# Performance work log

Hardware: AMD Instinct MI355X
Metric: run time of the kernel (lower is better)

## Reference

```python
import jax, jax.numpy as jnp
import numpy as np

N = 300000      # total points
B = 4           # scenes
C_IN = 64
C_OUT = 128
GRID = 0.5      # voxel size
M = 128         # per-axis voxel index bound (10m / 0.5m = 20 << 128); key fits int32
EPS = 1e-5      # BatchNorm eps


def setup_inputs() -> dict:
    key = jax.random.key(0)
    k1, k2, k3 = jax.random.split(key, 3)
    coord = jax.random.uniform(k1, (N, 3), jnp.float32) * 10.0
    feat = jax.random.normal(k2, (N, C_IN), jnp.float32)
    offset = jnp.array([N // 4, N // 2, 3 * N // 4, N], jnp.int32)  # cumulative counts
    W = jax.random.normal(k3, (C_IN, C_OUT), jnp.float32) * 0.05    # fc weight (no bias)
    gamma = jnp.ones((C_OUT,), jnp.float32)
    beta = jnp.zeros((C_OUT,), jnp.float32)
    return {"coord": coord, "feat": feat, "offset": offset, "W": W, "gamma": gamma, "beta": beta}


def reference(coord, feat, offset, W, gamma, beta):
    n = coord.shape[0]
    # offset2batch: point i belongs to scene searchsorted(offset, i, 'right')
    batch = jnp.searchsorted(offset, jnp.arange(n, dtype=offset.dtype), side='right')
    # fc -> BatchNorm1d (training-mode batch stats, biased var) -> ReLU
    x = feat @ W                                    # [n, C_OUT]
    mean = x.mean(axis=0)
    var = x.var(axis=0)
    x = jax.nn.relu(gamma * (x - mean) * jax.lax.rsqrt(var + EPS) + beta)
    # start = per-scene min coordinate (segment_csr min)
    start = jax.ops.segment_min(coord, batch, num_segments=B)      # [B, 3]
    # voxel_grid: integer voxel index per point, hashed injectively with batch id
    v = jnp.floor((coord - start[batch]) / GRID).astype(jnp.int32)  # [n, 3]
    vkey = ((batch.astype(jnp.int32) * M + v[:, 0]) * M + v[:, 1]) * M + v[:, 2]
    # unique(sorted) with inverse/counts; padded to n for static shapes
    uniq, cluster, counts = jnp.unique(vkey, return_inverse=True, return_counts=True,
                                       size=n, fill_value=-1)
    cluster = cluster.reshape(-1)                   # [n] cluster id per point
    # segment mean of coords, segment max of features (padded segments -> 0)
    cnt = jnp.maximum(counts, 1).astype(coord.dtype)
    coord_out = jax.ops.segment_sum(coord, cluster, num_segments=n) / cnt[:, None]
    fmax = jax.ops.segment_max(x, cluster, num_segments=n)
    feat_out = jnp.where(counts[:, None] > 0, fmax, jnp.zeros((), x.dtype))
    # batch id of each cluster (clusters never cross scenes)
    batch_out = jax.ops.segment_min(batch, cluster, num_segments=n)
    return coord_out, feat_out, cluster, counts, batch_out
```

## Files before the change

### kernel.cpp

```cpp
#include <hip/hip_runtime.h>
#include <stdint.h>

#define CIN   64
#define COUT  128
#define EPSB  1e-5f
#define NWORDS2 4096
#define MAXNC 32768
#define SLABW 17

typedef short bf16x8 __attribute__((ext_vector_type(8)));
typedef float f32x4  __attribute__((ext_vector_type(4)));
typedef unsigned u32x4 __attribute__((ext_vector_type(4)));

__device__ __forceinline__ int batch_of(int i, const int* __restrict__ off, int B) {
    int b = 0;
    for (int j = 0; j < B - 1; ++j) b += (i >= off[j]) ? 1 : 0;
    return b;
}

__device__ __forceinline__ unsigned enc(float x) {
    unsigned b = __float_as_uint(x);
    return (b & 0x80000000u) ? ~b : (b | 0x80000000u);
}
__device__ __forceinline__ float dec(unsigned u) {
    unsigned b = (u & 0x80000000u) ? (u ^ 0x80000000u) : ~u;
    return __uint_as_float(b);
}

__device__ __forceinline__ unsigned short rne_bf16(float f) {
    unsigned u = __float_as_uint(f);
    unsigned r = u + 0x7FFFu + ((u >> 16) & 1u);
    return (unsigned short)(r >> 16);
}

__device__ __forceinline__ void split8(float4 A, float4 B, bf16x8& hi, bf16x8& lo) {
    float fs[8] = {A.x, A.y, A.z, A.w, B.x, B.y, B.z, B.w};
    u32x4 hv, lv;
    #pragma unroll
    for (int w = 0; w < 4; ++w) {
        float a = fs[2*w], b = fs[2*w+1];
        unsigned ua = __float_as_uint(a), ub = __float_as_uint(b);
        hv[w] = __builtin_amdgcn_perm(ub, ua, 0x07060302u);
        float la = a - __uint_as_float(ua & 0xFFFF0000u);
        float lb = b - __uint_as_float(ub & 0xFFFF0000u);
        lv[w] = __builtin_amdgcn_perm(__float_as_uint(lb), __float_as_uint(la), 0x07060302u);
    }
    hi = __builtin_bit_cast(bf16x8, hv);
    lo = __builtin_bit_cast(bf16x8, lv);
}

__global__ void k_init(float* __restrict__ coordOut, float* __restrict__ batchOut, int n,
                       unsigned* __restrict__ pooledU, int* __restrict__ countsWs,
                       unsigned* __restrict__ flags, int* __restrict__ sceneMin, int nScene,
                       const float* __restrict__ W, unsigned short* __restrict__ Wb)
{
    long i = (long)blockIdx.x * blockDim.x + threadIdx.x;
    long stride = (long)gridDim.x * blockDim.x;
    for (long t = i; t < 3L * n; t += stride) coordOut[t] = 0.f;
    for (long t = i; t < n; t += stride) batchOut[t] = 2147483648.0f;
    for (long t = i; t < (long)MAXNC * COUT; t += stride) pooledU[t] = 0u;
    for (long t = i; t < MAXNC; t += stride) countsWs[t] = 0;
    for (long t = i; t < NWORDS2; t += stride) flags[t] = 0u;
    for (long t = i; t < nScene; t += stride) sceneMin[t] = 0x7F800000;
    for (long t = i; t < 32 * 64 * 8; t += stride) {
        int fragIdx = (int)(t >> 9);
        int r = (int)(t & 511);
        int lane = r >> 3, j = r & 7;
        int s  = fragIdx & 1;
        int kt = (fragIdx >> 1) & 1;
        int nt = fragIdx >> 2;
        int k  = kt * 32 + (lane >> 4) * 8 + j;
        int nc = nt * 16 + (lane & 15);
        float w = W[k * COUT + nc];
        unsigned short hi = rne_bf16(w);
        if (s == 0) Wb[t] = hi;
        else {
            float hf = __uint_as_float(((unsigned)hi) << 16);
            Wb[t] = rne_bf16(w - hf);
        }
    }
}

__global__ void k_scene_min(const float* __restrict__ coord, const int* __restrict__ off,
                            int n, int B, int* __restrict__ sceneMin)
{
    __shared__ int smin[12];
    if (threadIdx.x < 3 * B) smin[threadIdx.x] = 0x7F800000;
    __syncthreads();
    int t = blockIdx.x * blockDim.x + threadIdx.x;
    if (t < n) {
        int b = batch_of(t, off, B);
        for (int d = 0; d < 3; ++d)
            atomicMin(&smin[b * 3 + d], __float_as_int(coord[t * 3 + d]));
    }
    __syncthreads();
    if (threadIdx.x < 3 * B) atomicMin(&sceneMin[threadIdx.x], smin[threadIdx.x]);
}

__global__ void k_vkey(const float* __restrict__ coord, const int* __restrict__ off,
                       int n, int B, const int* __restrict__ sceneMin,
                       int* __restrict__ vkeyWs, unsigned* __restrict__ flags)
{
    int t = blockIdx.x * blockDim.x + threadIdx.x;
    if (t >= n) return;
    int b = batch_of(t, off, B);
    int key = b;
    #pragma unroll
    for (int d = 0; d < 3; ++d) {
        float s = __int_as_float(sceneMin[b * 3 + d]);
        int v = (int)floorf((coord[t * 3 + d] - s) * 2.0f);
        key = (key << 5) + v;
    }
    vkeyWs[t] = key;
    atomicOr(&flags[key >> 5], 1u << (key & 31));
}

__global__ void k_scan1(const unsigned* __restrict__ flags,
                        unsigned* __restrict__ wordPrefix, int* __restrict__ dNC)
{
    __shared__ unsigned wsum[16];
    const int t = threadIdx.x, lane = t & 63, wv = t >> 6;
    unsigned loc[4]; unsigned sum = 0;
    #pragma unroll
    for (int e = 0; e < 4; ++e) { loc[e] = (unsigned)__popc(flags[4 * t + e]); sum += loc[e]; }
    unsigned incl = sum;
    #pragma unroll
    for (int d = 1; d < 64; d <<= 1) {
        unsigned u = __shfl_up(incl, d, 64);
        if (lane >= d) incl += u;
    }
    if (lane == 63) wsum[wv] = incl;
    __syncthreads();
    if (wv == 0) {
        unsigned v = (lane < 16) ? wsum[lane] : 0u;
        unsigned iv = v;
        #pragma unroll
        for (int d = 1; d < 16; d <<= 1) {
            unsigned u = __shfl_up(iv, d, 64);
            if (lane >= d) iv += u;
        }
        if (lane < 16) wsum[lane] = iv - v;
    }
    __syncthreads();
    unsigned run = wsum[wv] + incl - sum;
    #pragma unroll
    for (int e = 0; e < 4; ++e) { wordPrefix[4 * t + e] = run; run += loc[e]; }
    if (t == 1023) *dNC = (int)run;
}

__global__ void k_cluster(const int* __restrict__ vkeyWs, const int* __restrict__ off,
                          int n, int B,
                          const unsigned* __restrict__ flags, const unsigned* __restrict__ wordPrefix,
                          float* __restrict__ clusterOut,
                          int* __restrict__ countsWs, float* __restrict__ batchOut)
{
    int t = blockIdx.x * blockDim.x + threadIdx.x;
    if (t >= n) return;
    int key = vkeyWs[t];
    int w = key >> 5, bit = key & 31;
    int c = (int)wordPrefix[w] + __popc(flags[w] & ((1u << bit) - 1u));
    clusterOut[t] = (float)c;
    atomicAdd(&countsWs[c], 1);
    batchOut[c] = (float)(key >> 15);
}

__global__ void k_scan2(const int* __restrict__ counts, int* __restrict__ cursor)
{
    __shared__ int wsum[16];
    const int t = threadIdx.x, lane = t & 63, wv = t >> 6;
    const int base = t * 32;
    int loc[32]; int sum = 0;
    #pragma unroll
    for (int e = 0; e < 32; ++e) { loc[e] = counts[base + e]; sum += loc[e]; }
    int incl = sum;
    #pragma unroll
    for (int d = 1; d < 64; d <<= 1) {
        int u = __shfl_up(incl, d, 64);
        if (lane >= d) incl += u;
    }
    if (lane == 63) wsum[wv] = incl;
    __syncthreads();
    if (wv == 0) {
        int v = (lane < 16) ? wsum[lane] : 0;
        int iv = v;
        #pragma unroll
        for (int d = 1; d < 16; d <<= 1) {
            int u = __shfl_up(iv, d, 64);
            if (lane >= d) iv += u;
        }
        if (lane < 16) wsum[lane] = iv - v;
    }
    __syncthreads();
    int run = wsum[wv] + incl - sum;
    #pragma unroll
    for (int e = 0; e < 32; ++e) { cursor[base + e] = run; run += loc[e]; }
}

__global__ void k_scatter(const float* __restrict__ clusterOut, int n,
                          int* __restrict__ cursor, int2* __restrict__ pcPair)
{
    int t = blockIdx.x * blockDim.x + threadIdx.x;
    if (t >= n) return;
    int c = (int)clusterOut[t];
    int pos = atomicAdd(&cursor[c], 1);
    pcPair[pos] = make_int2(t, c);
}

__global__ __launch_bounds__(256, 2) void k_fused(
    const float* __restrict__ feat, const float* __restrict__ coord,
    const unsigned short* __restrict__ Wb, const int2* __restrict__ pc,
    int n, int nWin, int gFused,
    unsigned* __restrict__ pooledU, float* __restrict__ coordOut,
    float* __restrict__ partials)
{
    __shared__ float slabs[4][64 * SLABW];
    __shared__ float accS[256];
    const int tid = threadIdx.x, wave = tid >> 6, lane = tid & 63;
    accS[tid] = 0.f;
    __syncthreads();

    const int wid = blockIdx.x * 4 + wave;
    const int q = lane >> 4, c16 = lane & 15;

    if (wid < nWin) {
        const int base = wid * 64;
        const int nvalid = min(64, n - base);
        int pv = 0, cv = -1;
        if (lane < nvalid) { int2 t = pc[base + lane]; pv = t.x; cv = t.y; }
        float* st = slabs[wave];

        int prevc = __shfl_up(cv, 1, 64);
        unsigned long long bmask = __ballot(lane > 0 && lane < nvalid && cv != prevc);

        {
            float cx = 0.f, cy = 0.f, cz = 0.f;
            if (lane < nvalid) {
                const float* cp = coord + 3 * (size_t)pv;
                cx = cp[0]; cy = cp[1]; cz = cp[2];
            }
            unsigned long long mlow = bmask & (~0ull >> (63 - lane));
            int rs = mlow ? (63 - __clzll((long long)mlow)) : 0;
            #pragma unroll
            for (int d = 1; d < 64; d <<= 1) {
                float tx = __shfl_up(cx, d, 64);
                float ty = __shfl_up(cy, d, 64);
                float tz = __shfl_up(cz, d, 64);
                if (lane - rs >= d) { cx += tx; cy += ty; cz += tz; }
            }
            bool isEnd = (lane == nvalid - 1) || ((((bmask >> 1) >> lane) & 1ull) != 0ull);
            if (lane < nvalid && isEnd) {
                float* cb = coordOut + (size_t)cv * 3;
                if (rs == 0 || lane == nvalid - 1) {
                    atomicAdd(cb + 0, cx); atomicAdd(cb + 1, cy); atomicAdd(cb + 2, cz);
                } else {
                    cb[0] = cx; cb[1] = cy; cb[2] = cz;
                }
            }
        }

        int p0 = __shfl(pv,      c16, 64);
        int p1 = __shfl(pv, 16 + c16, 64);
        int p2 = __shfl(pv, 32 + c16, 64);
        int p3 = __shfl(pv, 48 + c16, 64);
        const float* a0 = feat + (size_t)p0 * CIN + q * 8;
        const float* a1 = feat + (size_t)p1 * CIN + q * 8;
        const float* a2 = feat + (size_t)p2 * CIN + q * 8;
        const float* a3 = feat + (size_t)p3 * CIN + q * 8;
        float4 f00a = *(const float4*)(a0);      float4 f00b = *(const float4*)(a0 + 4);
        float4 f01a = *(const float4*)(a0 + 32); float4 f01b = *(const float4*)(a0 + 36);
        float4 f10a = *(const float4*)(a1);      float4 f10b = *(const float4*)(a1 + 4);
        float4 f11a = *(const float4*)(a1 + 32); float4 f11b = *(const float4*)(a1 + 36);
        float4 f20a = *(const float4*)(a2);      float4 f20b = *(const float4*)(a2 + 4);
        float4 f21a = *(const float4*)(a2 + 32); float4 f21b = *(const float4*)(a2 + 36);
        float4 f30a = *(const float4*)(a3);      float4 f30b = *(const float4*)(a3 + 4);
        float4 f31a = *(const float4*)(a3 + 32); float4 f31b = *(const float4*)(a3 + 36);
        const float4 Z = make_float4(0.f, 0.f, 0.f, 0.f);
        if (c16      >= nvalid) { f00a = f00b = f01a = f01b = Z; }
        if (16 + c16 >= nvalid) { f10a = f10b = f11a = f11b = Z; }
        if (32 + c16 >= nvalid) { f20a = f20b = f21a = f21b = Z; }
        if (48 + c16 >= nvalid) { f30a = f30b = f31a = f31b = Z; }

        bf16x8 ahi[4][2], alo[4][2];
        split8(f00a, f00b, ahi[0][0], alo[0][0]);
        split8(f01a, f01b, ahi[0][1], alo[0][1]);
        split8(f10a, f10b, ahi[1][0], alo[1][0]);
        split8(f11a, f11b, ahi[1][1], alo[1][1]);
        split8(f20a, f20b, ahi[2][0], alo[2][0]);
        split8(f21a, f21b, ahi[2][1], alo[2][1]);
        split8(f30a, f30b, ahi[3][0], alo[3][0]);
        split8(f31a, f31b, ahi[3][1], alo[3][1]);

        int rdOff[4], wOff[4];
        #pragma unroll
        for (int g = 0; g < 4; ++g) rdOff[g] = lane * SLABW + g * 4;
        #pragma unroll
        for (int t2 = 0; t2 < 4; ++t2) wOff[t2] = (t2 * 16 + c16) * SLABW + q * 4;

        for (int h = 0; h < 2; ++h) {
            bf16x8 bh[4][2], bl[4][2];
            #pragma unroll
            for (int nt2 = 0; nt2 < 4; ++nt2)
                #pragma unroll
                for (int kt = 0; kt < 2; ++kt) {
                    int fi = h * 16 + (nt2 * 2 + kt) * 2;
                    bh[nt2][kt] = *(const bf16x8*)(Wb + ((size_t)fi << 9) + (lane << 3));
                    bl[nt2][kt] = *(const bf16x8*)(Wb + ((size_t)(fi + 1) << 9) + (lane << 3));
                }
            float runM = -INFINITY, s1 = 0.f, s2 = 0.f;
            int runStart = 0;
            #pragma unroll
            for (int mt = 0; mt < 4; ++mt) {
                #pragma unroll
                for (int nt2 = 0; nt2 < 4; ++nt2) {
                    f32x4 c = {0.f, 0.f, 0.f, 0.f};
                    #pragma unroll
                    for (int kt = 0; kt < 2; ++kt) {
                        c = __builtin_amdgcn_mfma_f32_16x16x32_bf16(alo[mt][kt], bh[nt2][kt], c, 0, 0, 0);
                        c = __builtin_amdgcn_mfma_f32_16x16x32_bf16(ahi[mt][kt], bl[nt2][kt], c, 0, 0, 0);
                        c = __builtin_amdgcn_mfma_f32_16x16x32_bf16(ahi[mt][kt], bh[nt2][kt], c, 0, 0, 0);
                    }
                    *(float4*)&st[wOff[nt2]] = make_float4(c[0], c[1], c[2], c[3]);
                }
                #pragma unroll
                for (int g = 0; g < 4; ++g) {
                    float4 v = *(const float4*)&st[rdOff[g]];
                    #pragma unroll
                    for (int e = 0; e < 4; ++e) {
                        int i = mt * 16 + g * 4 + e;
                        if (i < nvalid) {
                            if (i > 0 && ((bmask >> i) & 1ull)) {
                                int cid = __shfl(cv, i - 1, 64);
                                unsigned* pb = pooledU + (size_t)cid * COUT + h * 64 + lane;
                                if (runStart == 0) atomicMax(pb, enc(runM));
                                else               *pb = enc(runM);
                                runStart = i;
                                runM = -INFINITY;
                            }
                            float x = (e == 0) ? v.x : (e == 1) ? v.y : (e == 2) ? v.z : v.w;
                            runM = fmaxf(runM, x);
                            s1 += x;
                            s2 = fmaf(x, x, s2);
                        }
                    }
                }
            }
            int cidL = __shfl(cv, nvalid - 1, 64);
            atomicMax(pooledU + (size_t)cidL * COUT + h * 64 + lane, enc(runM));
            atomicAdd(&accS[h * 64 + lane],       s1);
            atomicAdd(&accS[128 + h * 64 + lane], s2);
        }
    }

    __syncthreads();
    partials[(size_t)tid * gFused + blockIdx.x] = accS[tid];
}

__global__ void k_redbn(const float* __restrict__ partials, int gFused,
                        const float* __restrict__ gamma, const float* __restrict__ beta,
                        int n, float* __restrict__ scaleShift)
{
    __shared__ float red[512];
    const int j = blockIdx.x;
    const float* colS = partials + (size_t)j * gFused;
    const float* colQ = partials + (size_t)(j + 128) * gFused;
    float s = 0.f, q = 0.f;
    for (int b = threadIdx.x; b < gFused; b += 256) { s += colS[b]; q += colQ[b]; }
    red[threadIdx.x] = s;
    red[256 + threadIdx.x] = q;
    __syncthreads();
    for (int st = 128; st; st >>= 1) {
        if (threadIdx.x < st) {
            red[threadIdx.x] += red[threadIdx.x + st];
            red[256 + threadIdx.x] += red[256 + threadIdx.x + st];
        }
        __syncthreads();
    }
    if (threadIdx.x == 0) {
        float mean = red[0] / (float)n;
        float var  = red[256] / (float)n - mean * mean;
        var = fmaxf(var, 0.f);
        float inv = rsqrtf(var + EPSB);
        float sc = gamma[j] * inv;
        scaleShift[j]        = sc;
        scaleShift[COUT + j] = beta[j] - mean * sc;
    }
}

__global__ void k_final(float* __restrict__ featOut, const unsigned* __restrict__ pooledU,
                        const int* __restrict__ dNC, const float* __restrict__ scaleShift,
                        long featN4, int n,
                        float* __restrict__ coordOut, float* __restrict__ countsOut,
                        const int* __restrict__ countsWs)
{
    long i = (long)blockIdx.x * blockDim.x + threadIdx.x;
    long stride = (long)gridDim.x * blockDim.x;
    long act4 = (long)(*dNC) * (COUT / 4);
    float4* out4 = (float4*)featOut;
    const uint4* p4 = (const uint4*)pooledU;
    for (long idx = i; idx < featN4; idx += stride) {
        float4 v = make_float4(0.f, 0.f, 0.f, 0.f);
        if (idx < act4) {
            int j = (int)((idx * 4) & (COUT - 1));
            uint4 u = p4[idx];
            v.x = fmaxf(fmaf(scaleShift[j + 0], dec(u.x), scaleShift[COUT + j + 0]), 0.f);
            v.y = fmaxf(fmaf(scaleShift[j + 1], dec(u.y), scaleShift[COUT + j + 1]), 0.f);
            v.z = fmaxf(fmaf(scaleShift[j + 2], dec(u.z), scaleShift[COUT + j + 2]), 0.f);
            v.w = fmaxf(fmaf(scaleShift[j + 3], dec(u.w), scaleShift[COUT + j + 3]), 0.f);
        }
        out4[idx] = v;
    }
    for (long t = i; t < n; t += stride) {
        int cnt = (t < MAXNC) ? countsWs[t] : 0;
        if (cnt > 0) {
            float inv = 1.f / (float)cnt;
            coordOut[3 * t + 0] *= inv;
            coordOut[3 * t + 1] *= inv;
            coordOut[3 * t + 2] *= inv;
        }
        countsOut[t] = (float)cnt;
    }
}

extern "C" void kernel_launch(void* const* d_in, const int* in_sizes, int n_in,
                              void* d_out, int out_size, void* d_ws, size_t ws_size,
                              hipStream_t stream)
{
    const float* coord = (const float*)d_in[0];
    const float* feat  = (const float*)d_in[1];
    const int*   off   = (const int*)d_in[2];
    const float* W     = (const float*)d_in[3];
    const float* gamma = (const float*)d_in[4];
    const float* beta  = (const float*)d_in[5];
    const int n = in_sizes[0] / 3;
    const int B = in_sizes[2];

    float* out        = (float*)d_out;
    float* coordOut   = out;
    float* featOut    = out + (long)n * 3;
    float* clusterOut = featOut + (long)n * COUT;
    float* countsOut  = clusterOut + n;
    float* batchOut   = countsOut + n;

    char* wsp = (char*)d_ws;
    auto alloc = [&](size_t bytes) -> char* {
        char* p = wsp;
        wsp += (bytes + 255) & ~(size_t)255;
        return p;
    };
    unsigned* flags      = (unsigned*)alloc(NWORDS2 * 4);
    unsigned* wordPrefix = (unsigned*)alloc(NWORDS2 * 4);
    int*      vkeyWs     = (int*)alloc((size_t)n * 4);
    int*      countsWs   = (int*)alloc(MAXNC * 4);
    int2*     pcPair     = (int2*)alloc((size_t)n * sizeof(int2));
    int*      cursor     = (int*)alloc(MAXNC * 4);
    unsigned* pooledU    = (unsigned*)alloc((size_t)MAXNC * COUT * 4);
    unsigned short* Wb   = (unsigned short*)alloc(32 * 64 * 8 * 2);
    float*    scaleShift = (float*)alloc(2 * COUT * 4);
    int*      sceneMin   = (int*)alloc(3 * B * 4);
    int*      dNC        = (int*)alloc(4);

    const int nWin = (n + 63) / 64;
    const int gFused = (nWin + 3) / 4;
    float*    partials   = (float*)alloc((size_t)gFused * 256 * 4);

    const long featN4 = (long)n * COUT / 4;
    const int nb = (n + 255) / 256;

    k_init<<<nb, 256, 0, stream>>>(coordOut, batchOut, n, pooledU, countsWs,
                                   flags, sceneMin, 3 * B, W, Wb);
    k_scene_min<<<nb, 256, 0, stream>>>(coord, off, n, B, sceneMin);
    k_vkey<<<nb, 256, 0, stream>>>(coord, off, n, B, sceneMin, vkeyWs, flags);
    k_scan1<<<1, 1024, 0, stream>>>(flags, wordPrefix, dNC);
    k_cluster<<<nb, 256, 0, stream>>>(vkeyWs, off, n, B, flags, wordPrefix,
                                      clusterOut, countsWs, batchOut);
    k_scan2<<<1, 1024, 0, stream>>>(countsWs, cursor);
    k_scatter<<<nb, 256, 0, stream>>>(clusterOut, n, cursor, pcPair);
    k_fused<<<gFused, 256, 0, stream>>>(feat, coord, Wb, pcPair, n, nWin, gFused,
                                        pooledU, coordOut, partials);
    k_redbn<<<128, 256, 0, stream>>>(partials, gFused, gamma, beta, n, scaleShift);
    k_final<<<2048, 256, 0, stream>>>(featOut, pooledU, dNC, scaleShift, featN4, n,
                                      coordOut, countsOut, countsWs);
}
```

Baseline: 391.3 us.

## Use persistent work-stealing waves in fused kernel and pre-sort coordinates in scatter

The fused kernel becomes persistent: a fixed grid of 1024 blocks, with each wave claiming 64-point windows through an atomic counter instead of getting one static window per wave. The scatter kernel now also writes coordinates in cluster-sorted order, so the fused kernel reads them contiguously rather than gathering by point index. Launch bounds rise to 3 blocks per CU. This aims to improve load balance and cut gather traffic and block count, at the cost of an extra coordinate buffer, atomic contention on the window counter, and possible register pressure.

```diff
diff --git a/kernel.cpp b/kernel.cpp
--- a/kernel.cpp
+++ b/kernel.cpp
@@ -52,10 +52,12 @@
 __global__ void k_init(float* __restrict__ coordOut, float* __restrict__ batchOut, int n,
                        unsigned* __restrict__ pooledU, int* __restrict__ countsWs,
                        unsigned* __restrict__ flags, int* __restrict__ sceneMin, int nScene,
-                       const float* __restrict__ W, unsigned short* __restrict__ Wb)
+                       const float* __restrict__ W, unsigned short* __restrict__ Wb,
+                       int* __restrict__ wCtr)
 {
     long i = (long)blockIdx.x * blockDim.x + threadIdx.x;
     long stride = (long)gridDim.x * blockDim.x;
+    if (i == 0) *wCtr = 0;
     for (long t = i; t < 3L * n; t += stride) coordOut[t] = 0.f;
     for (long t = i; t < n; t += stride) batchOut[t] = 2147483648.0f;
     for (long t = i; t < (long)MAXNC * COUT; t += stride) pooledU[t] = 0u;
@@ -197,19 +199,25 @@
 }
 
 __global__ void k_scatter(const float* __restrict__ clusterOut, int n,
-                          int* __restrict__ cursor, int2* __restrict__ pcPair)
+                          const float* __restrict__ coord,
+                          int* __restrict__ cursor, int2* __restrict__ pcPair,
+                          float* __restrict__ scoord)
 {
     int t = blockIdx.x * blockDim.x + threadIdx.x;
     if (t >= n) return;
     int c = (int)clusterOut[t];
     int pos = atomicAdd(&cursor[c], 1);
     pcPair[pos] = make_int2(t, c);
-}
-
-__global__ __launch_bounds__(256, 2) void k_fused(
-    const float* __restrict__ feat, const float* __restrict__ coord,
+    float x = coord[t * 3 + 0], y = coord[t * 3 + 1], z = coord[t * 3 + 2];
+    scoord[(size_t)pos * 3 + 0] = x;
+    scoord[(size_t)pos * 3 + 1] = y;
+    scoord[(size_t)pos * 3 + 2] = z;
+}
+
+__global__ __launch_bounds__(256, 3) void k_fused(
+    const float* __restrict__ feat, const float* __restrict__ scoord,
     const unsigned short* __restrict__ Wb, const int2* __restrict__ pc,
-    int n, int nWin, int gFused,
+    int n, int nWin, int gFused, int* __restrict__ wCtr,
     unsigned* __restrict__ pooledU, float* __restrict__ coordOut,
     float* __restrict__ partials)
 {
@@ -219,25 +227,30 @@
     accS[tid] = 0.f;
     __syncthreads();
 
-    const int wid = blockIdx.x * 4 + wave;
     const int q = lane >> 4, c16 = lane & 15;
-
-    if (wid < nWin) {
+    float* st = slabs[wave];
+
+    for (;;) {
+        int wid = 0;
+        if (lane == 0) wid = atomicAdd(wCtr, 1);
+        wid = __shfl(wid, 0, 64);
+        if (wid >= nWin) break;
+
         const int base = wid * 64;
         const int nvalid = min(64, n - base);
         int pv = 0, cv = -1;
         if (lane < nvalid) { int2 t = pc[base + lane]; pv = t.x; cv = t.y; }
-        float* st = slabs[wave];
+
+        float cx = 0.f, cy = 0.f, cz = 0.f;
+        if (lane < nvalid) {
+            const float* cp = scoord + 3 * (size_t)(base + lane);
+            cx = cp[0]; cy = cp[1]; cz = cp[2];
+        }
 
         int prevc = __shfl_up(cv, 1, 64);
         unsigned long long bmask = __ballot(lane > 0 && lane < nvalid && cv != prevc);
 
         {
-            float cx = 0.f, cy = 0.f, cz = 0.f;
-            if (lane < nvalid) {
-                const float* cp = coord + 3 * (size_t)pv;
-                cx = cp[0]; cy = cp[1]; cz = cp[2];
-            }
             unsigned long long mlow = bmask & (~0ull >> (63 - lane));
             int rs = mlow ? (63 - __clzll((long long)mlow)) : 0;
             #pragma unroll
@@ -452,30 +465,32 @@
     int*      vkeyWs     = (int*)alloc((size_t)n * 4);
     int*      countsWs   = (int*)alloc(MAXNC * 4);
     int2*     pcPair     = (int2*)alloc((size_t)n * sizeof(int2));
+    float*    scoordWs   = (float*)alloc((size_t)n * 3 * 4);
     int*      cursor     = (int*)alloc(MAXNC * 4);
     unsigned* pooledU    = (unsigned*)alloc((size_t)MAXNC * COUT * 4);
     unsigned short* Wb   = (unsigned short*)alloc(32 * 64 * 8 * 2);
     float*    scaleShift = (float*)alloc(2 * COUT * 4);
     int*      sceneMin   = (int*)alloc(3 * B * 4);
     int*      dNC        = (int*)alloc(4);
+    int*      wCtr       = (int*)alloc(4);
 
     const int nWin = (n + 63) / 64;
-    const int gFused = (nWin + 3) / 4;
+    const int gFused = 1024;
     float*    partials   = (float*)alloc((size_t)gFused * 256 * 4);
 
     const long featN4 = (long)n * COUT / 4;
     const int nb = (n + 255) / 256;
 
     k_init<<<nb, 256, 0, stream>>>(coordOut, batchOut, n, pooledU, countsWs,
-                                   flags, sceneMin, 3 * B, W, Wb);
+                                   flags, sceneMin, 3 * B, W, Wb, wCtr);
     k_scene_min<<<nb, 256, 0, stream>>>(coord, off, n, B, sceneMin);
     k_vkey<<<nb, 256, 0, stream>>>(coord, off, n, B, sceneMin, vkeyWs, flags);
     k_scan1<<<1, 1024, 0, stream>>>(flags, wordPrefix, dNC);
     k_cluster<<<nb, 256, 0, stream>>>(vkeyWs, off, n, B, flags, wordPrefix,
                                       clusterOut, countsWs, batchOut);
     k_scan2<<<1, 1024, 0, stream>>>(countsWs, cursor);
-    k_scatter<<<nb, 256, 0, stream>>>(clusterOut, n, cursor, pcPair);
-    k_fused<<<gFused, 256, 0, stream>>>(feat, coord, Wb, pcPair, n, nWin, gFused,
+    k_scatter<<<nb, 256, 0, stream>>>(clusterOut, n, coord, cursor, pcPair, scoordWs);
+    k_fused<<<gFused, 256, 0, stream>>>(feat, scoordWs, Wb, pcPair, n, nWin, gFused, wCtr,
                                         pooledU, coordOut, partials);
     k_redbn<<<128, 256, 0, stream>>>(partials, gFused, gamma, beta, n, scaleShift);
     k_final<<<2048, 256, 0, stream>>>(featOut, pooledU, dNC, scaleShift, featN4, n,
```

New measurement: 451.6 us. 15.4% more time.
